# Kernel optimization log

Hardware: AMD Instinct MI355X
Metric: run time of the kernel (lower is better)

The kernel has to match this reference:

```python
import jax, jax.numpy as jnp
import numpy as np

FT_IN = 49152   # HalfKA feature space
VFT_IN = 768    # virtual (factored) feature space
FT_OUT = 512
BATCH = 8192
MAX_FEATS = 32  # max active features (pieces) per position
NNZ = BATCH * MAX_FEATS


def setup_inputs() -> dict:
    key = jax.random.key(0)
    ks = jax.random.split(key, 9)
    bidx = jnp.repeat(jnp.arange(BATCH, dtype=jnp.int64), MAX_FEATS)
    stm_feat = jax.random.randint(ks[0], (NNZ,), 0, FT_IN, dtype=jnp.int64)
    nstm_feat = jax.random.randint(ks[1], (NNZ,), 0, FT_IN, dtype=jnp.int64)
    stm_indices = jnp.stack([bidx, stm_feat])    # [2, nnz]
    nstm_indices = jnp.stack([bidx, nstm_feat])  # [2, nnz]
    values = jnp.ones((NNZ,), dtype=jnp.float32)
    s = 1.0 / np.sqrt(FT_IN)
    sv = 1.0 / np.sqrt(VFT_IN)
    so = 1.0 / np.sqrt(2 * FT_OUT)
    return {
        "stm_indices": stm_indices,
        "nstm_indices": nstm_indices,
        "values": values,
        "size": BATCH,
        "W_ft": jax.random.uniform(ks[2], (FT_IN, FT_OUT), jnp.float32, -s, s),
        "b_ft": jax.random.uniform(ks[3], (FT_OUT,), jnp.float32, -s, s),
        "W_fft": jax.random.uniform(ks[4], (VFT_IN, FT_OUT), jnp.float32, -sv, sv),
        "b_fft": jax.random.uniform(ks[5], (VFT_IN if False else FT_OUT,), jnp.float32, -sv, sv),
        "W_out": jax.random.uniform(ks[6], (2 * FT_OUT, 1), jnp.float32, -so, so),
        "b_out": jax.random.uniform(ks[7], (1,), jnp.float32, -so, so),
    }


def _perspective_ft(indices, values, size, W_ft, b_ft, W_fft, b_fft):
    # sparse feature-transformer: sum over active features of
    # (W_ft[f] + W_fft[f % 768]) * value, per batch row.
    bidx = indices[0]
    feat = indices[1]
    rows = values[:, None] * (W_ft[feat] + W_fft[feat % VFT_IN])  # [nnz, ft_out]
    acc = jax.ops.segment_sum(rows, bidx, num_segments=size)       # [B, ft_out]
    return acc + b_ft + b_fft


def reference(stm_indices, nstm_indices, values, size,
              W_ft, b_ft, W_fft, b_fft, W_out, b_out):
    stm_ft = _perspective_ft(stm_indices, values, size, W_ft, b_ft, W_fft, b_fft)
    nstm_ft = _perspective_ft(nstm_indices, values, size, W_ft, b_ft, W_fft, b_fft)
    hidden = jnp.clip(jnp.concatenate([stm_ft, nstm_ft], axis=1), 0.0, 1.0)
    return jax.nn.sigmoid(hidden @ W_out + b_out)  # [B, 1]
```

## Files before the change

### kernel.cpp

```cpp
#include <hip/hip_runtime.h>
#include <math.h>

#define MAXF   32
#define FTOUT  512
#define VFT    768
#define FTIN   49152
#define NCHUNK 8
#define RPB    32

__global__ __launch_bounds__(256)
void build_q8(const float* __restrict__ W_ft,
              const float* __restrict__ W_fft,
              unsigned char* __restrict__ Wq,
              float* __restrict__ scale)
{
    const int f    = blockIdx.x * 4 + (threadIdx.x >> 6);
    const int lane = threadIdx.x & 63;
    const long long rb = (long long)f * FTOUT + lane * 8;
    const float4 a0 = *(const float4*)(W_ft + rb);
    const float4 a1 = *(const float4*)(W_ft + rb + 4);
    const int fv = f % VFT;
    const float4 c0 = *(const float4*)(W_fft + fv * FTOUT + lane * 8);
    const float4 c1 = *(const float4*)(W_fft + fv * FTOUT + lane * 8 + 4);
    float w[8] = {a0.x+c0.x, a0.y+c0.y, a0.z+c0.z, a0.w+c0.w,
                  a1.x+c1.x, a1.y+c1.y, a1.z+c1.z, a1.w+c1.w};
    float m = fabsf(w[0]);
    #pragma unroll
    for (int t = 1; t < 8; ++t) m = fmaxf(m, fabsf(w[t]));
    #pragma unroll
    for (int s = 1; s < 64; s <<= 1) m = fmaxf(m, __shfl_xor(m, s));
    const float inv = (m > 0.f) ? 127.f / m : 0.f;
    if (lane == 0) scale[f] = (m > 0.f) ? m * (1.f / 127.f) : 0.f;
    unsigned u[8];
    #pragma unroll
    for (int t = 0; t < 8; ++t)
        u[t] = (unsigned)((int)rintf(w[t] * inv) + 128);
    uint2 o;
    o.x = u[0] | (u[1] << 8) | (u[2] << 16) | (u[3] << 24);
    o.y = u[4] | (u[5] << 8) | (u[6] << 16) | (u[7] << 24);
    *(uint2*)(Wq + (long long)f * FTOUT + lane * 8) = o;
}

__global__ __launch_bounds__(256)
void prep_idx(const int* __restrict__ stm_idx,
              const int* __restrict__ nstm_idx,
              const float* __restrict__ values,
              const float* __restrict__ scale,
              unsigned short* __restrict__ off16,
              float* __restrict__ val_s,
              float* __restrict__ val_n,
              int nnz, int batch)
{
    const int t = blockIdx.x * 256 + threadIdx.x;
    if (t >= batch * 64) return;
    const int b = t >> 6;
    const int k = t & 63;
    const int g = b * MAXF + (k & 31);
    const int f = (k < 32 ? stm_idx : nstm_idx)[nnz + g];
    off16[t] = (unsigned short)f;
    const float vs = values[g] * scale[f];
    if (k < 32) val_s[b * 32 + k] = vs;
    else        val_n[b * 32 + (k - 32)] = vs;
}

#define CONS_U8(A, W, V) do {                                     \
    A[0] = fmaf(V, (float)((W).x & 0xffu),         A[0]);         \
    A[1] = fmaf(V, (float)(((W).x >> 8)  & 0xffu), A[1]);         \
    A[2] = fmaf(V, (float)(((W).x >> 16) & 0xffu), A[2]);         \
    A[3] = fmaf(V, (float)((W).x >> 24),           A[3]);         \
    A[4] = fmaf(V, (float)((W).y & 0xffu),         A[4]);         \
    A[5] = fmaf(V, (float)(((W).y >> 8)  & 0xffu), A[5]);         \
    A[6] = fmaf(V, (float)(((W).y >> 16) & 0xffu), A[6]);         \
    A[7] = fmaf(V, (float)((W).y >> 24),           A[7]);         \
} while (0)

__global__ __launch_bounds__(256, 4)
void gather_q8(const unsigned char* __restrict__ Wq,
               const unsigned short* __restrict__ off16,
               const float* __restrict__ val_s,
               const float* __restrict__ val_n,
               const float* __restrict__ b_ft,
               const float* __restrict__ b_fft,
               const float* __restrict__ W_out,
               float* __restrict__ partial,
               int batch)
{
    const int c    = blockIdx.x & (NCHUNK - 1);
    const int rg   = blockIdx.x >> 3;
    const int tid  = threadIdx.x;
    const int wid  = tid >> 6;
    const int lane = tid & 63;
    const int r    = lane >> 5;
    const int fg   = (lane >> 3) & 3;
    const int cg   = lane & 7;

    __shared__ int   s_off[RPB][64];
    __shared__ float s_vs[RPB][32];
    __shared__ float s_vn[RPB][32];

    const int row_base = rg * RPB;

    {
        const unsigned* src = (const unsigned*)(off16 + row_base * 64);
        const unsigned p0 = src[tid * 4 + 0];
        const unsigned p1 = src[tid * 4 + 1];
        const unsigned p2 = src[tid * 4 + 2];
        const unsigned p3 = src[tid * 4 + 3];
        int* so = (int*)s_off;
        so[tid * 8 + 0] = (int)(p0 & 0xffffu) << 9;
        so[tid * 8 + 1] = (int)(p0 >> 16)     << 9;
        so[tid * 8 + 2] = (int)(p1 & 0xffffu) << 9;
        so[tid * 8 + 3] = (int)(p1 >> 16)     << 9;
        so[tid * 8 + 4] = (int)(p2 & 0xffffu) << 9;
        so[tid * 8 + 5] = (int)(p2 >> 16)     << 9;
        so[tid * 8 + 6] = (int)(p3 & 0xffffu) << 9;
        so[tid * 8 + 7] = (int)(p3 >> 16)     << 9;
        ((float4*)s_vs)[tid] = ((const float4*)(val_s + row_base * 32))[tid];
        ((float4*)s_vn)[tid] = ((const float4*)(val_n + row_base * 32))[tid];
    }
    __syncthreads();

    const int col = c * 64 + cg * 8;
    float bbq[8], wos[8], won[8];
    {
        const float4 a0 = *(const float4*)(b_ft + col);
        const float4 a1 = *(const float4*)(b_ft + col + 4);
        const float4 f0 = *(const float4*)(b_fft + col);
        const float4 f1 = *(const float4*)(b_fft + col + 4);
        bbq[0]=(a0.x+f0.x)*0.25f; bbq[1]=(a0.y+f0.y)*0.25f;
        bbq[2]=(a0.z+f0.z)*0.25f; bbq[3]=(a0.w+f0.w)*0.25f;
        bbq[4]=(a1.x+f1.x)*0.25f; bbq[5]=(a1.y+f1.y)*0.25f;
        bbq[6]=(a1.z+f1.z)*0.25f; bbq[7]=(a1.w+f1.w)*0.25f;
        const float4 s0 = *(const float4*)(W_out + col);
        const float4 s1 = *(const float4*)(W_out + col + 4);
        const float4 n0 = *(const float4*)(W_out + FTOUT + col);
        const float4 n1 = *(const float4*)(W_out + FTOUT + col + 4);
        wos[0]=s0.x; wos[1]=s0.y; wos[2]=s0.z; wos[3]=s0.w;
        wos[4]=s1.x; wos[5]=s1.y; wos[6]=s1.z; wos[7]=s1.w;
        won[0]=n0.x; won[1]=n0.y; won[2]=n0.z; won[3]=n0.w;
        won[4]=n1.x; won[5]=n1.y; won[6]=n1.z; won[7]=n1.w;
    }

    const char* wb = (const char*)Wq;
    const unsigned colb = (unsigned)(c * 64 + cg * 8);

    #pragma unroll
    for (int it = 0; it < 4; ++it) {
        const int lrow  = wid * 8 + 2 * it + r;
        const int row_g = row_base + lrow;

        const int*   po = &s_off[lrow][fg];
        const float* ps = &s_vs[lrow][fg];
        const float* pn = &s_vn[lrow][fg];

        const int o0 = po[0],  o1 = po[4],  o2 = po[8],  o3 = po[12];
        const int o4 = po[16], o5 = po[20], o6 = po[24], o7 = po[28];
        const int q0 = po[32], q1 = po[36], q2 = po[40], q3 = po[44];
        const int q4 = po[48], q5 = po[52], q6 = po[56], q7 = po[60];
        const float vs0 = ps[0],  vs1 = ps[4],  vs2 = ps[8],  vs3 = ps[12];
        const float vs4 = ps[16], vs5 = ps[20], vs6 = ps[24], vs7 = ps[28];
        const float vn0 = pn[0],  vn1 = pn[4],  vn2 = pn[8],  vn3 = pn[12];
        const float vn4 = pn[16], vn5 = pn[20], vn6 = pn[24], vn7 = pn[28];

        const uint2 a0 = *(const uint2*)(wb + (unsigned)o0 + colb);
        const uint2 a1 = *(const uint2*)(wb + (unsigned)o1 + colb);
        const uint2 a2 = *(const uint2*)(wb + (unsigned)o2 + colb);
        const uint2 a3 = *(const uint2*)(wb + (unsigned)o3 + colb);
        const uint2 a4 = *(const uint2*)(wb + (unsigned)o4 + colb);
        const uint2 a5 = *(const uint2*)(wb + (unsigned)o5 + colb);
        const uint2 a6 = *(const uint2*)(wb + (unsigned)o6 + colb);
        const uint2 a7 = *(const uint2*)(wb + (unsigned)o7 + colb);
        const uint2 b0 = *(const uint2*)(wb + (unsigned)q0 + colb);
        const uint2 b1 = *(const uint2*)(wb + (unsigned)q1 + colb);
        const uint2 b2 = *(const uint2*)(wb + (unsigned)q2 + colb);
        const uint2 b3 = *(const uint2*)(wb + (unsigned)q3 + colb);
        const uint2 b4 = *(const uint2*)(wb + (unsigned)q4 + colb);
        const uint2 b5 = *(const uint2*)(wb + (unsigned)q5 + colb);
        const uint2 b6 = *(const uint2*)(wb + (unsigned)q6 + colb);
        const uint2 b7 = *(const uint2*)(wb + (unsigned)q7 + colb);
        __builtin_amdgcn_sched_barrier(0);

        const float corr_s = 128.f * (((vs0+vs1)+(vs2+vs3)) + ((vs4+vs5)+(vs6+vs7)));
        const float corr_n = 128.f * (((vn0+vn1)+(vn2+vn3)) + ((vn4+vn5)+(vn6+vn7)));

        float acc_s[8], acc_n[8];
        #pragma unroll
        for (int t = 0; t < 8; ++t) {
            acc_s[t] = bbq[t] - corr_s;
            acc_n[t] = bbq[t] - corr_n;
        }

        CONS_U8(acc_s, a0, vs0); CONS_U8(acc_s, a1, vs1);
        CONS_U8(acc_s, a2, vs2); CONS_U8(acc_s, a3, vs3);
        CONS_U8(acc_s, a4, vs4); CONS_U8(acc_s, a5, vs5);
        CONS_U8(acc_s, a6, vs6); CONS_U8(acc_s, a7, vs7);
        CONS_U8(acc_n, b0, vn0); CONS_U8(acc_n, b1, vn1);
        CONS_U8(acc_n, b2, vn2); CONS_U8(acc_n, b3, vn3);
        CONS_U8(acc_n, b4, vn4); CONS_U8(acc_n, b5, vn5);
        CONS_U8(acc_n, b6, vn6); CONS_U8(acc_n, b7, vn7);

        #pragma unroll
        for (int t = 0; t < 8; ++t) {
            acc_s[t] += __shfl_xor(acc_s[t], 8);
            acc_n[t] += __shfl_xor(acc_n[t], 8);
        }
        #pragma unroll
        for (int t = 0; t < 8; ++t) {
            acc_s[t] += __shfl_xor(acc_s[t], 16);
            acc_n[t] += __shfl_xor(acc_n[t], 16);
        }

        float part = 0.f;
        #pragma unroll
        for (int t = 0; t < 8; ++t) {
            const float hs = fminf(fmaxf(acc_s[t], 0.f), 1.f);
            part = fmaf(hs, wos[t], part);
        }
        #pragma unroll
        for (int t = 0; t < 8; ++t) {
            const float hn = fminf(fmaxf(acc_n[t], 0.f), 1.f);
            part = fmaf(hn, won[t], part);
        }
        part += __shfl_xor(part, 1);
        part += __shfl_xor(part, 2);
        part += __shfl_xor(part, 4);

        if ((lane & 31) == 0 && row_g < batch)
            partial[row_g * NCHUNK + c] = part;
    }
}

__global__ __launch_bounds__(256)
void final_out(const float* __restrict__ partial,
               const float* __restrict__ b_out,
               float* __restrict__ out, int batch)
{
    const int b = blockIdx.x * 256 + threadIdx.x;
    if (b >= batch) return;
    const float4 p0 = *(const float4*)(partial + b * NCHUNK);
    const float4 p1 = *(const float4*)(partial + b * NCHUNK + 4);
    const float tot = ((p0.x + p0.y) + (p0.z + p0.w))
                    + ((p1.x + p1.y) + (p1.z + p1.w)) + b_out[0];
    out[b] = 1.0f / (1.0f + expf(-tot));
}

__global__ __launch_bounds__(256)
void nnhalfka_fused(const int* __restrict__ stm_idx,
                    const int* __restrict__ nstm_idx,
                    const float* __restrict__ values,
                    const float* __restrict__ W_ft,
                    const float* __restrict__ b_ft,
                    const float* __restrict__ W_fft,
                    const float* __restrict__ b_fft,
                    const float* __restrict__ W_out,
                    const float* __restrict__ b_out,
                    float* __restrict__ out,
                    int nnz)
{
    const int b   = blockIdx.x;
    const int tid = threadIdx.x;

    __shared__ int   s_fs[MAXF], s_fsm[MAXF], s_fn[MAXF], s_fnm[MAXF];
    __shared__ float s_v[MAXF];
    __shared__ float s_red[4];

    if (tid < MAXF) {
        const int g  = b * MAXF + tid;
        const int fs = stm_idx[nnz + g];
        const int fn = nstm_idx[nnz + g];
        s_fs[tid]  = fs * FTOUT;
        s_fsm[tid] = (fs % VFT) * FTOUT;
        s_fn[tid]  = fn * FTOUT;
        s_fnm[tid] = (fn % VFT) * FTOUT;
        s_v[tid]   = values[g];
    }
    __syncthreads();

    const int j = tid * 2;
    float2 accs = make_float2(0.f, 0.f);
    float2 accn = make_float2(0.f, 0.f);

    #pragma unroll 4
    for (int k = 0; k < MAXF; ++k) {
        const float v    = s_v[k];
        const float2 ws  = *(const float2*)(W_ft  + s_fs[k]  + j);
        const float2 wfs = *(const float2*)(W_fft + s_fsm[k] + j);
        const float2 wn  = *(const float2*)(W_ft  + s_fn[k]  + j);
        const float2 wfn = *(const float2*)(W_fft + s_fnm[k] + j);
        accs.x += v * (ws.x + wfs.x);
        accs.y += v * (ws.y + wfs.y);
        accn.x += v * (wn.x + wfn.x);
        accn.y += v * (wn.y + wfn.y);
    }

    const float bb0 = b_ft[j]     + b_fft[j];
    const float bb1 = b_ft[j + 1] + b_fft[j + 1];
    const float hs0 = fminf(fmaxf(accs.x + bb0, 0.f), 1.f);
    const float hs1 = fminf(fmaxf(accs.y + bb1, 0.f), 1.f);
    const float hn0 = fminf(fmaxf(accn.x + bb0, 0.f), 1.f);
    const float hn1 = fminf(fmaxf(accn.y + bb1, 0.f), 1.f);

    float partial = hs0 * W_out[j]         + hs1 * W_out[j + 1]
                  + hn0 * W_out[FTOUT + j] + hn1 * W_out[FTOUT + j + 1];
    #pragma unroll
    for (int off = 32; off > 0; off >>= 1)
        partial += __shfl_down(partial, off);
    if ((tid & 63) == 0) s_red[tid >> 6] = partial;
    __syncthreads();
    if (tid == 0) {
        const float tot = s_red[0] + s_red[1] + s_red[2] + s_red[3] + b_out[0];
        out[b] = 1.0f / (1.0f + expf(-tot));
    }
}

extern "C" void kernel_launch(void* const* d_in, const int* in_sizes, int n_in,
                              void* d_out, int out_size, void* d_ws, size_t ws_size,
                              hipStream_t stream) {
    const int*   stm_idx  = (const int*)d_in[0];
    const int*   nstm_idx = (const int*)d_in[1];
    const float* values   = (const float*)d_in[2];
    const float* W_ft     = (const float*)d_in[4];
    const float* b_ft     = (const float*)d_in[5];
    const float* W_fft    = (const float*)d_in[6];
    const float* b_fft    = (const float*)d_in[7];
    const float* W_out    = (const float*)d_in[8];
    const float* b_out    = (const float*)d_in[9];
    float* out = (float*)d_out;

    const int nnz   = in_sizes[0] / 2;
    const int batch = out_size;

    const size_t WQ_B   = (size_t)FTIN * FTOUT;
    const size_t SC_B   = (size_t)FTIN * 4;
    const size_t OFF_B  = (size_t)batch * 64 * 2;
    const size_t VS_B   = (size_t)batch * 32 * 4;
    const size_t VN_B   = (size_t)batch * 32 * 4;
    const size_t PART_B = (size_t)batch * NCHUNK * 4;
    const size_t need = WQ_B + SC_B + OFF_B + VS_B + VN_B + PART_B;

    if (ws_size >= need && (batch % RPB) == 0) {
        char* p = (char*)d_ws;
        unsigned char*  Wq      = (unsigned char*)p;        p += WQ_B;
        float*          scale   = (float*)p;                p += SC_B;
        unsigned short* off16   = (unsigned short*)p;       p += OFF_B;
        float*          val_s   = (float*)p;                p += VS_B;
        float*          val_n   = (float*)p;                p += VN_B;
        float*          partial = (float*)p;

        build_q8<<<FTIN / 4, 256, 0, stream>>>(W_ft, W_fft, Wq, scale);
        prep_idx<<<(batch * 64 + 255) / 256, 256, 0, stream>>>(
            stm_idx, nstm_idx, values, scale, off16, val_s, val_n, nnz, batch);
        gather_q8<<<(batch / RPB) * NCHUNK, 256, 0, stream>>>(
            Wq, off16, val_s, val_n, b_ft, b_fft, W_out, partial, batch);
        final_out<<<(batch + 255) / 256, 256, 0, stream>>>(partial, b_out, out, batch);
    } else {
        nnhalfka_fused<<<batch, 256, 0, stream>>>(
            stm_idx, nstm_idx, values, W_ft, b_ft, W_fft, b_fft, W_out, b_out,
            out, nnz);
    }
}
```

Baseline: 68.64 us.

## Software-pipeline gather loads across row iterations in gather_q8

Replaces the four-iteration row loop with a manually unrolled schedule. The weight gathers for the next row half are issued, behind sched_barrier fences, before the current row's dequantize-accumulate work, so global load latency overlaps with ALU work. This raises live register pressure, since up to three sets of 8 uint2 loads can be in flight at once, and that may reduce occupancy under launch_bounds(256,4). The row_g < batch guard on the partial store is also dropped.

```diff
diff --git a/kernel.cpp b/kernel.cpp
--- a/kernel.cpp
+++ b/kernel.cpp
@@ -74,6 +74,73 @@
     A[7] = fmaf(V, (float)((W).y >> 24),           A[7]);         \
 } while (0)
 
+#define GLD(OFF) (*(const uint2*)(wb + (unsigned)(OFF) + colb))
+
+#define META(T) \
+    const int lrow##T = wid * 8 + 2 * (T) + r; \
+    const int* po##T = &s_off[lrow##T][fg]; \
+    const float* ps##T = &s_vs[lrow##T][fg]; \
+    const float* pn##T = &s_vn[lrow##T][fg];
+
+#define LOAD_S(T) \
+    const uint2 sa##T##_0 = GLD(po##T[0]);  const uint2 sa##T##_1 = GLD(po##T[4]); \
+    const uint2 sa##T##_2 = GLD(po##T[8]);  const uint2 sa##T##_3 = GLD(po##T[12]); \
+    const uint2 sa##T##_4 = GLD(po##T[16]); const uint2 sa##T##_5 = GLD(po##T[20]); \
+    const uint2 sa##T##_6 = GLD(po##T[24]); const uint2 sa##T##_7 = GLD(po##T[28]); \
+    __builtin_amdgcn_sched_barrier(0);
+
+#define LOAD_N(T) \
+    const uint2 nb##T##_0 = GLD(po##T[32]); const uint2 nb##T##_1 = GLD(po##T[36]); \
+    const uint2 nb##T##_2 = GLD(po##T[40]); const uint2 nb##T##_3 = GLD(po##T[44]); \
+    const uint2 nb##T##_4 = GLD(po##T[48]); const uint2 nb##T##_5 = GLD(po##T[52]); \
+    const uint2 nb##T##_6 = GLD(po##T[56]); const uint2 nb##T##_7 = GLD(po##T[60]); \
+    __builtin_amdgcn_sched_barrier(0);
+
+#define CONS_S(T) \
+    const float vs##T##_0 = ps##T[0],  vs##T##_1 = ps##T[4],  vs##T##_2 = ps##T[8],  vs##T##_3 = ps##T[12]; \
+    const float vs##T##_4 = ps##T[16], vs##T##_5 = ps##T[20], vs##T##_6 = ps##T[24], vs##T##_7 = ps##T[28]; \
+    const float corr_s##T = 128.f * (((vs##T##_0+vs##T##_1)+(vs##T##_2+vs##T##_3)) + ((vs##T##_4+vs##T##_5)+(vs##T##_6+vs##T##_7))); \
+    float accs##T[8]; \
+    _Pragma("unroll") \
+    for (int t = 0; t < 8; ++t) accs##T[t] = bbq[t] - corr_s##T; \
+    CONS_U8(accs##T, sa##T##_0, vs##T##_0); CONS_U8(accs##T, sa##T##_1, vs##T##_1); \
+    CONS_U8(accs##T, sa##T##_2, vs##T##_2); CONS_U8(accs##T, sa##T##_3, vs##T##_3); \
+    CONS_U8(accs##T, sa##T##_4, vs##T##_4); CONS_U8(accs##T, sa##T##_5, vs##T##_5); \
+    CONS_U8(accs##T, sa##T##_6, vs##T##_6); CONS_U8(accs##T, sa##T##_7, vs##T##_7);
+
+#define CONS_N(T) \
+    const float vn##T##_0 = pn##T[0],  vn##T##_1 = pn##T[4],  vn##T##_2 = pn##T[8],  vn##T##_3 = pn##T[12]; \
+    const float vn##T##_4 = pn##T[16], vn##T##_5 = pn##T[20], vn##T##_6 = pn##T[24], vn##T##_7 = pn##T[28]; \
+    const float corr_n##T = 128.f * (((vn##T##_0+vn##T##_1)+(vn##T##_2+vn##T##_3)) + ((vn##T##_4+vn##T##_5)+(vn##T##_6+vn##T##_7))); \
+    float accn##T[8]; \
+    _Pragma("unroll") \
+    for (int t = 0; t < 8; ++t) accn##T[t] = bbq[t] - corr_n##T; \
+    CONS_U8(accn##T, nb##T##_0, vn##T##_0); CONS_U8(accn##T, nb##T##_1, vn##T##_1); \
+    CONS_U8(accn##T, nb##T##_2, vn##T##_2); CONS_U8(accn##T, nb##T##_3, vn##T##_3); \
+    CONS_U8(accn##T, nb##T##_4, vn##T##_4); CONS_U8(accn##T, nb##T##_5, vn##T##_5); \
+    CONS_U8(accn##T, nb##T##_6, vn##T##_6); CONS_U8(accn##T, nb##T##_7, vn##T##_7);
+
+#define EPI(T) { \
+    _Pragma("unroll") \
+    for (int t = 0; t < 8; ++t) { \
+        accs##T[t] += __shfl_xor(accs##T[t], 8); \
+        accn##T[t] += __shfl_xor(accn##T[t], 8); } \
+    _Pragma("unroll") \
+    for (int t = 0; t < 8; ++t) { \
+        accs##T[t] += __shfl_xor(accs##T[t], 16); \
+        accn##T[t] += __shfl_xor(accn##T[t], 16); } \
+    float part = 0.f; \
+    _Pragma("unroll") \
+    for (int t = 0; t < 8; ++t) \
+        part = fmaf(fminf(fmaxf(accs##T[t], 0.f), 1.f), wos[t], part); \
+    _Pragma("unroll") \
+    for (int t = 0; t < 8; ++t) \
+        part = fmaf(fminf(fmaxf(accn##T[t], 0.f), 1.f), won[t], part); \
+    part += __shfl_xor(part, 1); \
+    part += __shfl_xor(part, 2); \
+    part += __shfl_xor(part, 4); \
+    if ((lane & 31) == 0) partial[(row_base + lrow##T) * NCHUNK + c] = part; }
+
 __global__ __launch_bounds__(256, 4)
 void gather_q8(const unsigned char* __restrict__ Wq,
                const unsigned short* __restrict__ off16,
@@ -144,90 +211,28 @@
     const char* wb = (const char*)Wq;
     const unsigned colb = (unsigned)(c * 64 + cg * 8);
 
-    #pragma unroll
-    for (int it = 0; it < 4; ++it) {
-        const int lrow  = wid * 8 + 2 * it + r;
-        const int row_g = row_base + lrow;
-
-        const int*   po = &s_off[lrow][fg];
-        const float* ps = &s_vs[lrow][fg];
-        const float* pn = &s_vn[lrow][fg];
-
-        const int o0 = po[0],  o1 = po[4],  o2 = po[8],  o3 = po[12];
-        const int o4 = po[16], o5 = po[20], o6 = po[24], o7 = po[28];
-        const int q0 = po[32], q1 = po[36], q2 = po[40], q3 = po[44];
-        const int q4 = po[48], q5 = po[52], q6 = po[56], q7 = po[60];
-        const float vs0 = ps[0],  vs1 = ps[4],  vs2 = ps[8],  vs3 = ps[12];
-        const float vs4 = ps[16], vs5 = ps[20], vs6 = ps[24], vs7 = ps[28];
-        const float vn0 = pn[0],  vn1 = pn[4],  vn2 = pn[8],  vn3 = pn[12];
-        const float vn4 = pn[16], vn5 = pn[20], vn6 = pn[24], vn7 = pn[28];
-
-        const uint2 a0 = *(const uint2*)(wb + (unsigned)o0 + colb);
-        const uint2 a1 = *(const uint2*)(wb + (unsigned)o1 + colb);
-        const uint2 a2 = *(const uint2*)(wb + (unsigned)o2 + colb);
-        const uint2 a3 = *(const uint2*)(wb + (unsigned)o3 + colb);
-        const uint2 a4 = *(const uint2*)(wb + (unsigned)o4 + colb);
-        const uint2 a5 = *(const uint2*)(wb + (unsigned)o5 + colb);
-        const uint2 a6 = *(const uint2*)(wb + (unsigned)o6 + colb);
-        const uint2 a7 = *(const uint2*)(wb + (unsigned)o7 + colb);
-        const uint2 b0 = *(const uint2*)(wb + (unsigned)q0 + colb);
-        const uint2 b1 = *(const uint2*)(wb + (unsigned)q1 + colb);
-        const uint2 b2 = *(const uint2*)(wb + (unsigned)q2 + colb);
-        const uint2 b3 = *(const uint2*)(wb + (unsigned)q3 + colb);
-        const uint2 b4 = *(const uint2*)(wb + (unsigned)q4 + colb);
-        const uint2 b5 = *(const uint2*)(wb + (unsigned)q5 + colb);
-        const uint2 b6 = *(const uint2*)(wb + (unsigned)q6 + colb);
-        const uint2 b7 = *(const uint2*)(wb + (unsigned)q7 + colb);
-        __builtin_amdgcn_sched_barrier(0);
-
-        const float corr_s = 128.f * (((vs0+vs1)+(vs2+vs3)) + ((vs4+vs5)+(vs6+vs7)));
-        const float corr_n = 128.f * (((vn0+vn1)+(vn2+vn3)) + ((vn4+vn5)+(vn6+vn7)));
-
-        float acc_s[8], acc_n[8];
-        #pragma unroll
-        for (int t = 0; t < 8; ++t) {
-            acc_s[t] = bbq[t] - corr_s;
-            acc_n[t] = bbq[t] - corr_n;
-        }
-
-        CONS_U8(acc_s, a0, vs0); CONS_U8(acc_s, a1, vs1);
-        CONS_U8(acc_s, a2, vs2); CONS_U8(acc_s, a3, vs3);
-        CONS_U8(acc_s, a4, vs4); CONS_U8(acc_s, a5, vs5);
-        CONS_U8(acc_s, a6, vs6); CONS_U8(acc_s, a7, vs7);
-        CONS_U8(acc_n, b0, vn0); CONS_U8(acc_n, b1, vn1);
-        CONS_U8(acc_n, b2, vn2); CONS_U8(acc_n, b3, vn3);
-        CONS_U8(acc_n, b4, vn4); CONS_U8(acc_n, b5, vn5);
-        CONS_U8(acc_n, b6, vn6); CONS_U8(acc_n, b7, vn7);
-
-        #pragma unroll
-        for (int t = 0; t < 8; ++t) {
-            acc_s[t] += __shfl_xor(acc_s[t], 8);
-            acc_n[t] += __shfl_xor(acc_n[t], 8);
-        }
-        #pragma unroll
-        for (int t = 0; t < 8; ++t) {
-            acc_s[t] += __shfl_xor(acc_s[t], 16);
-            acc_n[t] += __shfl_xor(acc_n[t], 16);
-        }
-
-        float part = 0.f;
-        #pragma unroll
-        for (int t = 0; t < 8; ++t) {
-            const float hs = fminf(fmaxf(acc_s[t], 0.f), 1.f);
-            part = fmaf(hs, wos[t], part);
-        }
-        #pragma unroll
-        for (int t = 0; t < 8; ++t) {
-            const float hn = fminf(fmaxf(acc_n[t], 0.f), 1.f);
-            part = fmaf(hn, won[t], part);
-        }
-        part += __shfl_xor(part, 1);
-        part += __shfl_xor(part, 2);
-        part += __shfl_xor(part, 4);
-
-        if ((lane & 31) == 0 && row_g < batch)
-            partial[row_g * NCHUNK + c] = part;
-    }
+    META(0) META(1) META(2) META(3)
+
+    LOAD_S(0)
+    LOAD_N(0)
+    LOAD_S(1)
+    CONS_S(0)
+    LOAD_N(1)
+    CONS_N(0)
+    EPI(0)
+    LOAD_S(2)
+    CONS_S(1)
+    LOAD_N(2)
+    CONS_N(1)
+    EPI(1)
+    LOAD_S(3)
+    CONS_S(2)
+    LOAD_N(3)
+    CONS_N(2)
+    EPI(2)
+    CONS_S(3)
+    CONS_N(3)
+    EPI(3)
 }
 
 __global__ __launch_bounds__(256)
```

After: 69.39 us. No clear change (+1.1%).

## Assign one row per 8-lane group to drop cross-lane feature reductions

Applied to the files above, without the earlier changes.

Remaps gather_q8 work so each 8-lane group owns a whole row and loops over all 64 features itself. This removes the per-row shuffle reductions across feature groups and the 4-iteration row loop. The packed 16-bit offsets are now kept in padded shared memory and decoded per load, and the occupancy hint is raised to 6 blocks per SM. In exchange, each lane does a longer serial chain of dependent FMAs and issues fewer concurrent loads in flight per row.

```diff
diff --git a/kernel.cpp b/kernel.cpp
--- a/kernel.cpp
+++ b/kernel.cpp
@@ -74,7 +74,7 @@
     A[7] = fmaf(V, (float)((W).y >> 24),           A[7]);         \
 } while (0)
 
-__global__ __launch_bounds__(256, 4)
+__global__ __launch_bounds__(256, 6)
 void gather_q8(const unsigned char* __restrict__ Wq,
                const unsigned short* __restrict__ off16,
                const float* __restrict__ val_s,
@@ -90,47 +90,41 @@
     const int tid  = threadIdx.x;
     const int wid  = tid >> 6;
     const int lane = tid & 63;
-    const int r    = lane >> 5;
-    const int fg   = (lane >> 3) & 3;
+    const int ri   = lane >> 3;
     const int cg   = lane & 7;
 
-    __shared__ int   s_off[RPB][64];
-    __shared__ float s_vs[RPB][32];
-    __shared__ float s_vn[RPB][32];
+    __shared__ unsigned s_offp[RPB][33];
+    __shared__ float    s_val[RPB][66];
 
     const int row_base = rg * RPB;
 
     {
         const unsigned* src = (const unsigned*)(off16 + row_base * 64);
-        const unsigned p0 = src[tid * 4 + 0];
-        const unsigned p1 = src[tid * 4 + 1];
-        const unsigned p2 = src[tid * 4 + 2];
-        const unsigned p3 = src[tid * 4 + 3];
-        int* so = (int*)s_off;
-        so[tid * 8 + 0] = (int)(p0 & 0xffffu) << 9;
-        so[tid * 8 + 1] = (int)(p0 >> 16)     << 9;
-        so[tid * 8 + 2] = (int)(p1 & 0xffffu) << 9;
-        so[tid * 8 + 3] = (int)(p1 >> 16)     << 9;
-        so[tid * 8 + 4] = (int)(p2 & 0xffffu) << 9;
-        so[tid * 8 + 5] = (int)(p2 >> 16)     << 9;
-        so[tid * 8 + 6] = (int)(p3 & 0xffffu) << 9;
-        so[tid * 8 + 7] = (int)(p3 >> 16)     << 9;
-        ((float4*)s_vs)[tid] = ((const float4*)(val_s + row_base * 32))[tid];
-        ((float4*)s_vn)[tid] = ((const float4*)(val_n + row_base * 32))[tid];
+        #pragma unroll
+        for (int i = 0; i < 4; ++i) {
+            const int idx = i * 256 + tid;
+            s_offp[idx >> 5][idx & 31] = src[idx];
+        }
+        #pragma unroll
+        for (int i = 0; i < 8; ++i) {
+            const int idx = i * 256 + tid;
+            const int row = idx >> 6;
+            const int k   = idx & 63;
+            s_val[row][k] = (k < 32) ? val_s[(row_base + row) * 32 + k]
+                                     : val_n[(row_base + row) * 32 + (k - 32)];
+        }
     }
     __syncthreads();
 
     const int col = c * 64 + cg * 8;
-    float bbq[8], wos[8], won[8];
+    float bb[8], wos[8], won[8];
     {
         const float4 a0 = *(const float4*)(b_ft + col);
         const float4 a1 = *(const float4*)(b_ft + col + 4);
         const float4 f0 = *(const float4*)(b_fft + col);
         const float4 f1 = *(const float4*)(b_fft + col + 4);
-        bbq[0]=(a0.x+f0.x)*0.25f; bbq[1]=(a0.y+f0.y)*0.25f;
-        bbq[2]=(a0.z+f0.z)*0.25f; bbq[3]=(a0.w+f0.w)*0.25f;
-        bbq[4]=(a1.x+f1.x)*0.25f; bbq[5]=(a1.y+f1.y)*0.25f;
-        bbq[6]=(a1.z+f1.z)*0.25f; bbq[7]=(a1.w+f1.w)*0.25f;
+        bb[0]=a0.x+f0.x; bb[1]=a0.y+f0.y; bb[2]=a0.z+f0.z; bb[3]=a0.w+f0.w;
+        bb[4]=a1.x+f1.x; bb[5]=a1.y+f1.y; bb[6]=a1.z+f1.z; bb[7]=a1.w+f1.w;
         const float4 s0 = *(const float4*)(W_out + col);
         const float4 s1 = *(const float4*)(W_out + col + 4);
         const float4 n0 = *(const float4*)(W_out + FTOUT + col);
@@ -144,90 +138,54 @@
     const char* wb = (const char*)Wq;
     const unsigned colb = (unsigned)(c * 64 + cg * 8);
 
-    #pragma unroll
-    for (int it = 0; it < 4; ++it) {
-        const int lrow  = wid * 8 + 2 * it + r;
-        const int row_g = row_base + lrow;
-
-        const int*   po = &s_off[lrow][fg];
-        const float* ps = &s_vs[lrow][fg];
-        const float* pn = &s_vn[lrow][fg];
-
-        const int o0 = po[0],  o1 = po[4],  o2 = po[8],  o3 = po[12];
-        const int o4 = po[16], o5 = po[20], o6 = po[24], o7 = po[28];
-        const int q0 = po[32], q1 = po[36], q2 = po[40], q3 = po[44];
-        const int q4 = po[48], q5 = po[52], q6 = po[56], q7 = po[60];
-        const float vs0 = ps[0],  vs1 = ps[4],  vs2 = ps[8],  vs3 = ps[12];
-        const float vs4 = ps[16], vs5 = ps[20], vs6 = ps[24], vs7 = ps[28];
-        const float vn0 = pn[0],  vn1 = pn[4],  vn2 = pn[8],  vn3 = pn[12];
-        const float vn4 = pn[16], vn5 = pn[20], vn6 = pn[24], vn7 = pn[28];
-
-        const uint2 a0 = *(const uint2*)(wb + (unsigned)o0 + colb);
-        const uint2 a1 = *(const uint2*)(wb + (unsigned)o1 + colb);
-        const uint2 a2 = *(const uint2*)(wb + (unsigned)o2 + colb);
-        const uint2 a3 = *(const uint2*)(wb + (unsigned)o3 + colb);
-        const uint2 a4 = *(const uint2*)(wb + (unsigned)o4 + colb);
-        const uint2 a5 = *(const uint2*)(wb + (unsigned)o5 + colb);
-        const uint2 a6 = *(const uint2*)(wb + (unsigned)o6 + colb);
-        const uint2 a7 = *(const uint2*)(wb + (unsigned)o7 + colb);
-        const uint2 b0 = *(const uint2*)(wb + (unsigned)q0 + colb);
-        const uint2 b1 = *(const uint2*)(wb + (unsigned)q1 + colb);
-        const uint2 b2 = *(const uint2*)(wb + (unsigned)q2 + colb);
-        const uint2 b3 = *(const uint2*)(wb + (unsigned)q3 + colb);
-        const uint2 b4 = *(const uint2*)(wb + (unsigned)q4 + colb);
-        const uint2 b5 = *(const uint2*)(wb + (unsigned)q5 + colb);
-        const uint2 b6 = *(const uint2*)(wb + (unsigned)q6 + colb);
-        const uint2 b7 = *(const uint2*)(wb + (unsigned)q7 + colb);
-        __builtin_amdgcn_sched_barrier(0);
-
-        const float corr_s = 128.f * (((vs0+vs1)+(vs2+vs3)) + ((vs4+vs5)+(vs6+vs7)));
-        const float corr_n = 128.f * (((vn0+vn1)+(vn2+vn3)) + ((vn4+vn5)+(vn6+vn7)));
-
-        float acc_s[8], acc_n[8];
-        #pragma unroll
-        for (int t = 0; t < 8; ++t) {
-            acc_s[t] = bbq[t] - corr_s;
-            acc_n[t] = bbq[t] - corr_n;
-        }
-
-        CONS_U8(acc_s, a0, vs0); CONS_U8(acc_s, a1, vs1);
-        CONS_U8(acc_s, a2, vs2); CONS_U8(acc_s, a3, vs3);
-        CONS_U8(acc_s, a4, vs4); CONS_U8(acc_s, a5, vs5);
-        CONS_U8(acc_s, a6, vs6); CONS_U8(acc_s, a7, vs7);
-        CONS_U8(acc_n, b0, vn0); CONS_U8(acc_n, b1, vn1);
-        CONS_U8(acc_n, b2, vn2); CONS_U8(acc_n, b3, vn3);
-        CONS_U8(acc_n, b4, vn4); CONS_U8(acc_n, b5, vn5);
-        CONS_U8(acc_n, b6, vn6); CONS_U8(acc_n, b7, vn7);
-
-        #pragma unroll
-        for (int t = 0; t < 8; ++t) {
-            acc_s[t] += __shfl_xor(acc_s[t], 8);
-            acc_n[t] += __shfl_xor(acc_n[t], 8);
-        }
-        #pragma unroll
-        for (int t = 0; t < 8; ++t) {
-            acc_s[t] += __shfl_xor(acc_s[t], 16);
-            acc_n[t] += __shfl_xor(acc_n[t], 16);
-        }
-
-        float part = 0.f;
-        #pragma unroll
-        for (int t = 0; t < 8; ++t) {
-            const float hs = fminf(fmaxf(acc_s[t], 0.f), 1.f);
-            part = fmaf(hs, wos[t], part);
-        }
-        #pragma unroll
-        for (int t = 0; t < 8; ++t) {
-            const float hn = fminf(fmaxf(acc_n[t], 0.f), 1.f);
-            part = fmaf(hn, won[t], part);
-        }
-        part += __shfl_xor(part, 1);
-        part += __shfl_xor(part, 2);
-        part += __shfl_xor(part, 4);
-
-        if ((lane & 31) == 0 && row_g < batch)
-            partial[row_g * NCHUNK + c] = part;
-    }
+    const int row_l = wid * 8 + ri;
+    const int row_g = row_base + row_l;
+
+    float acc_s[8] = {0.f,0.f,0.f,0.f,0.f,0.f,0.f,0.f};
+    float acc_n[8] = {0.f,0.f,0.f,0.f,0.f,0.f,0.f,0.f};
+    float corr_s = 0.f, corr_n = 0.f;
+
+    #pragma unroll 4
+    for (int kk = 0; kk < 16; ++kk) {
+        const unsigned p = s_offp[row_l][kk];
+        const float2 v = *(const float2*)&s_val[row_l][2 * kk];
+        const uint2 w0 = *(const uint2*)(wb + ((p & 0xffffu) << 9) + colb);
+        const uint2 w1 = *(const uint2*)(wb + ((p >> 16) << 9) + colb);
+        corr_s += v.x + v.y;
+        CONS_U8(acc_s, w0, v.x);
+        CONS_U8(acc_s, w1, v.y);
+    }
+    #pragma unroll 4
+    for (int kk = 16; kk < 32; ++kk) {
+        const unsigned p = s_offp[row_l][kk];
+        const float2 v = *(const float2*)&s_val[row_l][2 * kk];
+        const uint2 w0 = *(const uint2*)(wb + ((p & 0xffffu) << 9) + colb);
+        const uint2 w1 = *(const uint2*)(wb + ((p >> 16) << 9) + colb);
+        corr_n += v.x + v.y;
+        CONS_U8(acc_n, w0, v.x);
+        CONS_U8(acc_n, w1, v.y);
+    }
+
+    const float cs = 128.f * corr_s;
+    const float cn = 128.f * corr_n;
+
+    float part = 0.f;
+    #pragma unroll
+    for (int t = 0; t < 8; ++t) {
+        const float hs = fminf(fmaxf(acc_s[t] - cs + bb[t], 0.f), 1.f);
+        part = fmaf(hs, wos[t], part);
+    }
+    #pragma unroll
+    for (int t = 0; t < 8; ++t) {
+        const float hn = fminf(fmaxf(acc_n[t] - cn + bb[t], 0.f), 1.f);
+        part = fmaf(hn, won[t], part);
+    }
+    part += __shfl_xor(part, 1);
+    part += __shfl_xor(part, 2);
+    part += __shfl_xor(part, 4);
+
+    if (cg == 0 && row_g < batch)
+        partial[row_g * NCHUNK + c] = part;
 }
 
 __global__ __launch_bounds__(256)
```

New measurement: 73.47 us. 7.0% more time.
